# Kernel optimization log

Measured on AMD Instinct MI355X. Metric: run time of the kernel, lower is better.

## Reference

```python
import jax, jax.numpy as jnp
import numpy as np

H, D = 16, 64  # num_head, num_out
LN_EPS = 1e-5

def setup_inputs() -> dict:
    key = jax.random.key(0)
    ks = jax.random.split(key, 6)
    B, S, C = 4, 2048, 1024
    sc = 0.02
    return {
        "x": jax.random.normal(ks[0], (B, S, C), jnp.float32),
        "mask": jax.random.randint(ks[1], (B, S), 0, 2, jnp.int32),
        "Wq": jax.random.normal(ks[2], (C, C), jnp.float32) * sc,
        "Wk": jax.random.normal(ks[3], (C, C), jnp.float32) * sc,
        "Wv": jax.random.normal(ks[4], (C, C), jnp.float32) * sc,
        "Wr": jax.random.normal(ks[5], (C, C), jnp.float32) * sc,
        "gamma": jnp.ones((C,), jnp.float32),
        "beta": jnp.zeros((C,), jnpip := jnp.float32) if False else jnp.zeros((C,), jnp.float32),
    }

def reference(x, mask, Wq, Wk, Wv, Wr, gamma, beta):
    B, S, C = x.shape
    # torch Linear: y = x @ W.T ; split(num_out,-1) == reshape (B,S,H,D)
    q = (x @ Wq.T).reshape(B, S, H, D)
    k = (x @ Wk.T).reshape(B, S, H, D)
    v = (x @ Wv.T).reshape(B, S, H, D)
    scores = jnp.einsum("bqhd,bkhd->bhqk", q, k) / jnp.sqrt(jnp.float32(D))
    # mask [B,S] over keys; masked positions -> -1e9 (matches masked_fill)
    scores = jnp.where((mask == 0)[:, None, None, :], jnp.float32(-1e9), scores)
    attn = jax.nn.softmax(scores, axis=-1)
    out = jnp.einsum("bhqk,bkhd->bqhd", attn, v).reshape(B, S, H * D)
    out = jax.nn.relu(out + x @ Wr.T)
    mu = jnp.mean(out, axis=-1, keepdims=True)
    var = jnp.mean(jnp.square(out - mu), axis=-1, keepdims=True)
    return (out - mu) / jnp.sqrt(var + LN_EPS) * gamma + beta
```

## Files before the change

### kernel.cpp

```cpp
#include <hip/hip_runtime.h>

typedef __attribute__((ext_vector_type(8))) short short8;
typedef __attribute__((ext_vector_type(4))) float f32x4;
typedef __attribute__((ext_vector_type(4))) unsigned short u16x4;
typedef __attribute__((ext_vector_type(4))) float float4v;

#define MFMA(a, b, c) __builtin_amdgcn_mfma_f32_16x16x32_bf16(a, b, c, 0, 0, 0)
#define GLOAD_LDS16(gp, lp) __builtin_amdgcn_global_load_lds( \
    (const __attribute__((address_space(1))) void*)(gp),      \
    (__attribute__((address_space(3))) void*)(lp), 16, 0, 0)

__device__ __forceinline__ float bf2f(unsigned short u) {
    union { unsigned int i; float f; } v; v.i = ((unsigned int)u) << 16; return v.f;
}
__device__ __forceinline__ unsigned short f2bf(float f) {
    union { float f; unsigned int i; } v; v.f = f;
    unsigned int r = (v.i + 0x7FFFu + ((v.i >> 16) & 1u)) >> 16;
    return (unsigned short)r;
}
__device__ __forceinline__ unsigned short f2bfr(float f) {
    union { float f; unsigned int i; } v; v.f = f;
    return (unsigned short)((v.i + 0x8000u) >> 16);
}

__global__ __launch_bounds__(256)
void mask_scan(const int* __restrict__ mask, int* __restrict__ kidx, int* __restrict__ seff)
{
    constexpr int S = 2048;
    const int b = blockIdx.x;
    const int tid = threadIdx.x;
    __shared__ int ps[256];
    const int* m = mask + b * S;
    int loc[8], s = 0;
#pragma unroll
    for (int j = 0; j < 8; ++j) { loc[j] = m[tid * 8 + j]; s += loc[j]; }
#pragma unroll
    for (int j = 0; j < 8; ++j) kidx[b * S + tid * 8 + j] = b * S;
    ps[tid] = s;
    __syncthreads();
    for (int off = 1; off < 256; off <<= 1) {
        int v = (tid >= off) ? ps[tid - off] : 0;
        __syncthreads();
        ps[tid] += v;
        __syncthreads();
    }
    int run = (tid > 0) ? ps[tid - 1] : 0;
#pragma unroll
    for (int j = 0; j < 8; ++j) {
        if (loc[j]) kidx[b * S + run] = b * S + tid * 8 + j;
        run += loc[j];
    }
    if (tid == 255) seff[b] = ps[255];
}

__global__ __launch_bounds__(256)
void ingest(const float* __restrict__ src, unsigned short* __restrict__ dst, int n4)
{
    const int stride = gridDim.x * blockDim.x;
    for (int i = blockIdx.x * blockDim.x + threadIdx.x; i < n4; i += stride) {
        float4v v = ((const float4v*)src)[i];
        u16x4 o;
#pragma unroll
        for (int j = 0; j < 4; ++j) o[j] = f2bf(v[j]);
        ((u16x4*)dst)[i] = o;
    }
}

__global__ __launch_bounds__(256)
void proj_gemm(const unsigned short* __restrict__ X,
               const unsigned short* __restrict__ Wq, const unsigned short* __restrict__ Wk,
               const unsigned short* __restrict__ Wv, const unsigned short* __restrict__ Wr,
               unsigned short* __restrict__ Qo, unsigned short* __restrict__ Ko,
               unsigned short* __restrict__ Vo, unsigned short* __restrict__ Ro,
               const int* __restrict__ kidx, const int* __restrict__ seff)
{
    constexpr int Kd = 1024, N = 1024;
    __shared__ unsigned short As[128 * 32];
    __shared__ unsigned short Bs[128 * 32];
    const int tid = threadIdx.x;
    const int wid = tid >> 6, lane = tid & 63;
    const int g = lane >> 4, lr = lane & 15;
    const int wsel = blockIdx.z;
    const bool compact = (wsel == 1) || (wsel == 2);
    int rowBase;
    if (compact) {
        int bx = blockIdx.x;
        int b = bx / 17, xt = bx - b * 17;
        if (xt * 128 >= seff[b]) return;
        rowBase = b * 2048 + xt * 128;
    } else {
        if (blockIdx.x >= 64) return;
        rowBase = blockIdx.x * 128;
    }
    const unsigned short* W = (wsel == 0) ? Wq : (wsel == 1) ? Wk : (wsel == 2) ? Wv : Wr;
    unsigned short* O = (wsel == 0) ? Qo : (wsel == 1) ? Ko : (wsel == 2) ? Vo : Ro;
    const int colBase = blockIdx.y * 128;
    const int wm = wid >> 1, wn = wid & 1;

    f32x4 acc[4][4] = {};

    const int r0 = tid >> 2;
    const int c0 = (tid & 3) * 8;
    const int sA0 = compact ? kidx[rowBase + r0] : rowBase + r0;
    const int sA1 = compact ? kidx[rowBase + 64 + r0] : rowBase + 64 + r0;
    const unsigned short* ga0 = X + (size_t)sA0 * Kd + c0;
    const unsigned short* ga1 = X + (size_t)sA1 * Kd + c0;
    const unsigned short* gb0 = W + (size_t)(colBase + r0) * Kd + c0;
    const unsigned short* gb1 = W + (size_t)(colBase + 64 + r0) * Kd + c0;

    for (int kt = 0; kt < Kd; kt += 32) {
        if (kt) __syncthreads();
        GLOAD_LDS16(ga0 + kt, As + (size_t)tid * 8);
        GLOAD_LDS16(ga1 + kt, As + 2048 + (size_t)tid * 8);
        GLOAD_LDS16(gb0 + kt, Bs + (size_t)tid * 8);
        GLOAD_LDS16(gb1 + kt, Bs + 2048 + (size_t)tid * 8);
        asm volatile("s_waitcnt vmcnt(0)" ::: "memory");
        __syncthreads();
        short8 a[4], b[4];
#pragma unroll
        for (int mt = 0; mt < 4; ++mt)
            a[mt] = *reinterpret_cast<const short8*>(&As[(wm * 64 + mt * 16 + lr) * 32 + g * 8]);
#pragma unroll
        for (int nt = 0; nt < 4; ++nt)
            b[nt] = *reinterpret_cast<const short8*>(&Bs[(wn * 64 + nt * 16 + lr) * 32 + g * 8]);
#pragma unroll
        for (int mt = 0; mt < 4; ++mt)
#pragma unroll
            for (int nt = 0; nt < 4; ++nt)
                acc[mt][nt] = MFMA(a[mt], b[nt], acc[mt][nt]);
    }
#pragma unroll
    for (int mt = 0; mt < 4; ++mt)
#pragma unroll
        for (int nt = 0; nt < 4; ++nt)
#pragma unroll
            for (int r = 0; r < 4; ++r) {
                int row = rowBase + wm * 64 + mt * 16 + g * 4 + r;
                int col = colBase + wn * 64 + nt * 16 + lr;
                O[(size_t)row * N + col] = f2bf(acc[mt][nt][r]);
            }
}

__global__ __launch_bounds__(512)
void attn_fwd(const unsigned short* __restrict__ Q, const unsigned short* __restrict__ Kb,
              const unsigned short* __restrict__ Vb, const int* __restrict__ seff,
              unsigned short* __restrict__ AO)
{
    constexpr int S = 2048, C = 1024, Dh = 64;
    constexpr int PST = 64;
    constexpr float SCL = 0.125f * 1.44269504f;
    constexpr float FM  = 16.0f;
    constexpr float MSK = -1.0e30f;
    __shared__ unsigned short Kt[2][64 * 64];
    __shared__ unsigned short Vt[2][64 * 64];
    __shared__ unsigned short Pt[8][16 * PST];
    const int tid = threadIdx.x;
    const int w = tid >> 6, lane = tid & 63;
    const int g = lane >> 4, lr = lane & 15;
    const int lin = blockIdx.x;
    const int hb = lin & 63, qt = lin >> 6;
    const int h = hb >> 2, b = hb & 3;
    const int qbase = qt * 128;
    const int qrow = qbase + w * 16 + lr;

    const int Sb = seff[b];
    const int ntiles = (Sb + 63) >> 6;

    const unsigned short* qptr = Q + (size_t)(b * S + qrow) * C + h * Dh;
    short8 qf[2];
    qf[0] = *reinterpret_cast<const short8*>(qptr + g * 8);
    qf[1] = *reinterpret_cast<const short8*>(qptr + 32 + g * 8);

    short8 ones;
#pragma unroll
    for (int j = 0; j < 8; ++j) ones[j] = (short)0x3F80;

    f32x4 o[4] = {};
    f32x4 lacc = {};

    const unsigned short* kg = Kb + (size_t)(b * S) * C + h * Dh;
    const unsigned short* vg = Vb + (size_t)(b * S) * C + h * Dh;

    const int kk0 = tid >> 3;
    const int kd0 = ((tid & 7) ^ (kk0 & 7)) * 8;
    const int vkey = tid >> 3;
    const int vsd = (tid & 7) * 8;

    short8 vv;
    GLOAD_LDS16(kg + (size_t)kk0 * C + kd0, &Kt[0][(size_t)tid * 8]);
    vv = *reinterpret_cast<const short8*>(vg + (size_t)vkey * C + vsd);
    asm volatile("s_waitcnt vmcnt(0)" ::: "memory");
    {
        const unsigned short* bb = (const unsigned short*)&vv;
#pragma unroll
        for (int j = 0; j < 8; ++j) {
            int d = vsd + j;
            int sw = (d & 7) ^ ((d >> 3) & 7);
            Vt[0][d * 64 + ((((vkey >> 3) ^ sw) << 3) | (vkey & 7))] = bb[j];
        }
    }
    __syncthreads();

    int cur = 0;
    for (int tt = 0; tt < ntiles; ++tt) {
        const int t = tt * 64;
        const bool hasNext = (tt + 1) < ntiles;
        if (hasNext) {
            const int tn = t + 64;
            GLOAD_LDS16(kg + (size_t)(tn + kk0) * C + kd0, &Kt[cur ^ 1][(size_t)tid * 8]);
            vv = *reinterpret_cast<const short8*>(vg + (size_t)(tn + vkey) * C + vsd);
        }
        f32x4 s[4];
        __builtin_amdgcn_s_setprio(1);
#pragma unroll
        for (int nt = 0; nt < 4; ++nt) {
            int key = nt * 16 + lr;
            f32x4 a = {};
#pragma unroll
            for (int c = 0; c < 2; ++c) {
                int dd = c * 32 + g * 8;
                short8 kf = *reinterpret_cast<const short8*>(
                    &Kt[cur][key * 64 + (((dd >> 3) ^ (key & 7)) << 3)]);
                a = MFMA(qf[c], kf, a);
            }
            s[nt] = a;
        }
        __builtin_amdgcn_s_setprio(0);
        float madd[4];
#pragma unroll
        for (int nt = 0; nt < 4; ++nt)
            madd[nt] = ((t + nt * 16 + lr) < Sb) ? -FM : MSK;
        unsigned short* Pw = Pt[w];
#pragma unroll
        for (int nt = 0; nt < 4; ++nt) {
            int k = nt * 16 + lr;
#pragma unroll
            for (int r = 0; r < 4; ++r) {
                float p = __builtin_amdgcn_exp2f(s[nt][r] * SCL + madd[nt]);
                int row = g * 4 + r;
                Pw[row * PST + ((((k >> 3) ^ (row & 7)) << 3) | (k & 7))] = f2bfr(p);
            }
        }
        asm volatile("s_waitcnt lgkmcnt(0)" ::: "memory");
        __builtin_amdgcn_sched_barrier(0);
        short8 pf[2];
#pragma unroll
        for (int hh = 0; hh < 2; ++hh) {
            int kk = hh * 32 + g * 8;
            pf[hh] = *reinterpret_cast<const short8*>(
                &Pw[lr * PST + (((kk >> 3) ^ (lr & 7)) << 3)]);
        }
        __builtin_amdgcn_s_setprio(1);
        lacc = MFMA(pf[0], ones, lacc);
        lacc = MFMA(pf[1], ones, lacc);
#pragma unroll
        for (int dt = 0; dt < 4; ++dt) {
            int d = dt * 16 + lr;
#pragma unroll
            for (int hh = 0; hh < 2; ++hh) {
                int kk = hh * 32 + g * 8;
                short8 vf = *reinterpret_cast<const short8*>(
                    &Vt[cur][d * 64 + ((((kk >> 3) ^ (d & 7) ^ ((d >> 3) & 7)) << 3))]);
                o[dt] = MFMA(pf[hh], vf, o[dt]);
            }
        }
        __builtin_amdgcn_s_setprio(0);
        if (hasNext) {
            asm volatile("s_waitcnt vmcnt(0)" ::: "memory");
            const unsigned short* bb = (const unsigned short*)&vv;
            unsigned short* Vn = Vt[cur ^ 1];
#pragma unroll
            for (int j = 0; j < 8; ++j) {
                int d = vsd + j;
                int sw = (d & 7) ^ ((d >> 3) & 7);
                Vn[d * 64 + ((((vkey >> 3) ^ sw) << 3) | (vkey & 7))] = bb[j];
            }
        }
        __syncthreads();
        cur ^= 1;
    }
#pragma unroll
    for (int dt = 0; dt < 4; ++dt)
#pragma unroll
        for (int r = 0; r < 4; ++r) {
            int row = qbase + w * 16 + g * 4 + r;
            int col = h * Dh + dt * 16 + lr;
            AO[(size_t)(b * S + row) * C + col] = f2bf(o[dt][r] / lacc[r]);
        }
}

__global__ __launch_bounds__(256)
void ln_ep(const unsigned short* __restrict__ AO, const unsigned short* __restrict__ R,
           const float* __restrict__ gamma, const float* __restrict__ beta,
           float* __restrict__ out)
{
    constexpr int C = 1024;
    const int row = blockIdx.x;
    const int tid = threadIdx.x;
    __shared__ float s1[256];
    __shared__ float s2[256];

    float v[4]; float sum = 0.f, ss = 0.f;
#pragma unroll
    for (int i = 0; i < 4; ++i) {
        int c = tid * 4 + i;
        float a = bf2f(AO[(size_t)row * C + c]);
        float r = bf2f(R[(size_t)row * C + c]);
        v[i] = fmaxf(0.f, a + r);
        sum += v[i]; ss += v[i] * v[i];
    }
    s1[tid] = sum; s2[tid] = ss;
    __syncthreads();
    for (int st = 128; st > 0; st >>= 1) {
        if (tid < st) { s1[tid] += s1[tid + st]; s2[tid] += s2[tid + st]; }
        __syncthreads();
    }
    float mu = s1[0] * (1.f / C);
    float var = s2[0] * (1.f / C) - mu * mu;
    float rstd = rsqrtf(var + 1e-5f);
    float4v g4 = *reinterpret_cast<const float4v*>(gamma + tid * 4);
    float4v b4 = *reinterpret_cast<const float4v*>(beta + tid * 4);
    float4v ov;
#pragma unroll
    for (int i = 0; i < 4; ++i)
        ov[i] = (v[i] - mu) * rstd * g4[i] + b4[i];
    *reinterpret_cast<float4v*>(out + (size_t)row * C + tid * 4) = ov;
}

extern "C" void kernel_launch(void* const* d_in, const int* in_sizes, int n_in,
                              void* d_out, int out_size, void* d_ws, size_t ws_size,
                              hipStream_t stream)
{
    const float* X = (const float*)d_in[0];
    const int* mask = (const int*)d_in[1];
    const float* Wq = (const float*)d_in[2];
    const float* Wk = (const float*)d_in[3];
    const float* Wv = (const float*)d_in[4];
    const float* Wr = (const float*)d_in[5];
    const float* Gm = (const float*)d_in[6];
    const float* Bt = (const float*)d_in[7];
    float* out = (float*)d_out;

    const size_t NE = (size_t)8192 * 1024;
    const size_t WE = (size_t)1024 * 1024;
    unsigned short* p = (unsigned short*)d_ws;
    unsigned short* Xb = p;   p += NE;
    unsigned short* Wqb = p;  p += WE;
    unsigned short* Wkb = p;  p += WE;
    unsigned short* Wvb = p;  p += WE;
    unsigned short* Wrb = p;  p += WE;
    unsigned short* Qb = p;   p += NE;
    unsigned short* Kb = p;   p += NE;
    unsigned short* Vb = p;   p += NE;
    unsigned short* Rb = p;   p += NE;
    int* kidx = (int*)p;      p += 8192 * 2;
    int* seff = (int*)p;      p += 8;
    unsigned short* AO = Xb;

    mask_scan<<<dim3(4), 256, 0, stream>>>(mask, kidx, seff);
    ingest<<<dim3(2048), 256, 0, stream>>>(X, Xb, (int)(NE / 4));
    ingest<<<dim3(512), 256, 0, stream>>>(Wq, Wqb, (int)(WE / 4));
    ingest<<<dim3(512), 256, 0, stream>>>(Wk, Wkb, (int)(WE / 4));
    ingest<<<dim3(512), 256, 0, stream>>>(Wv, Wvb, (int)(WE / 4));
    ingest<<<dim3(512), 256, 0, stream>>>(Wr, Wrb, (int)(WE / 4));

    proj_gemm<<<dim3(68, 8, 4), 256, 0, stream>>>(Xb, Wqb, Wkb, Wvb, Wrb,
                                                  Qb, Kb, Vb, Rb, kidx, seff);
    attn_fwd<<<dim3(1024), 512, 0, stream>>>(Qb, Kb, Vb, seff, AO);
    ln_ep<<<dim3(8192), 256, 0, stream>>>(AO, Rb, Gm, Bt, out);
}
```

Before: 177.2 us.

## Fuse ingest launches, swizzle projection grid, and coalesce GEMM stores via LDS

Merges the five fp32-to-bf16 conversion launches into one kernel writing the contiguous workspace. Flattens the projection GEMM grid to a 1D index grouped so eight row tiles share weight column tiles, aiming for better cache reuse. Stages the output tile through padded shared memory so global stores become 16-byte coalesced rows instead of scattered 2-byte writes. The extra shared buffer raises LDS use per block, which may lower occupancy.

```diff
diff --git a/kernel.cpp b/kernel.cpp
--- a/kernel.cpp
+++ b/kernel.cpp
@@ -1,6 +1,7 @@
 #include <hip/hip_runtime.h>
 
 typedef __attribute__((ext_vector_type(8))) short short8;
+typedef __attribute__((ext_vector_type(8))) unsigned short u16x8;
 typedef __attribute__((ext_vector_type(4))) float f32x4;
 typedef __attribute__((ext_vector_type(4))) unsigned short u16x4;
 typedef __attribute__((ext_vector_type(4))) float float4v;
@@ -54,11 +55,25 @@
 }
 
 __global__ __launch_bounds__(256)
-void ingest(const float* __restrict__ src, unsigned short* __restrict__ dst, int n4)
-{
+void ingest_all(const float* __restrict__ X,
+                const float* __restrict__ Wq, const float* __restrict__ Wk,
+                const float* __restrict__ Wv, const float* __restrict__ Wr,
+                unsigned short* __restrict__ dst)
+{
+    constexpr int X4 = 2097152;
+    constexpr int T4 = X4 + 4 * 262144;
     const int stride = gridDim.x * blockDim.x;
-    for (int i = blockIdx.x * blockDim.x + threadIdx.x; i < n4; i += stride) {
-        float4v v = ((const float4v*)src)[i];
+    for (int i = blockIdx.x * blockDim.x + threadIdx.x; i < T4; i += stride) {
+        const float* src;
+        int off;
+        if (i < X4) { src = X; off = i; }
+        else {
+            int jj = i - X4;
+            int ws = jj >> 18;
+            off = jj & 0x3FFFF;
+            src = (ws == 0) ? Wq : (ws == 1) ? Wk : (ws == 2) ? Wv : Wr;
+        }
+        float4v v = ((const float4v*)src)[off];
         u16x4 o;
 #pragma unroll
         for (int j = 0; j < 4; ++j) o[j] = f2bf(v[j]);
@@ -77,24 +92,30 @@
     constexpr int Kd = 1024, N = 1024;
     __shared__ unsigned short As[128 * 32];
     __shared__ unsigned short Bs[128 * 32];
+    __shared__ unsigned short Ct[128 * 136];
     const int tid = threadIdx.x;
     const int wid = tid >> 6, lane = tid & 63;
     const int g = lane >> 4, lr = lane & 15;
-    const int wsel = blockIdx.z;
+    const int bid = blockIdx.x;
+    const int jx = bid & 7, t = bid >> 3;
+    const int x = (t >> 5) * 8 + jx;
+    const int c = t & 31;
+    const int wsel = c >> 3;
+    const int coltile = c & 7;
     const bool compact = (wsel == 1) || (wsel == 2);
     int rowBase;
     if (compact) {
-        int bx = blockIdx.x;
-        int b = bx / 17, xt = bx - b * 17;
+        if (x >= 68) return;
+        int b = x / 17, xt = x - b * 17;
         if (xt * 128 >= seff[b]) return;
         rowBase = b * 2048 + xt * 128;
     } else {
-        if (blockIdx.x >= 64) return;
-        rowBase = blockIdx.x * 128;
+        if (x >= 64) return;
+        rowBase = x * 128;
     }
     const unsigned short* W = (wsel == 0) ? Wq : (wsel == 1) ? Wk : (wsel == 2) ? Wv : Wr;
     unsigned short* O = (wsel == 0) ? Qo : (wsel == 1) ? Ko : (wsel == 2) ? Vo : Ro;
-    const int colBase = blockIdx.y * 128;
+    const int colBase = coltile * 128;
     const int wm = wid >> 1, wn = wid & 1;
 
     f32x4 acc[4][4] = {};
@@ -134,11 +155,17 @@
 #pragma unroll
         for (int nt = 0; nt < 4; ++nt)
 #pragma unroll
-            for (int r = 0; r < 4; ++r) {
-                int row = rowBase + wm * 64 + mt * 16 + g * 4 + r;
-                int col = colBase + wn * 64 + nt * 16 + lr;
-                O[(size_t)row * N + col] = f2bf(acc[mt][nt][r]);
-            }
+            for (int r = 0; r < 4; ++r)
+                Ct[(wm * 64 + mt * 16 + g * 4 + r) * 136 + wn * 64 + nt * 16 + lr] =
+                    f2bf(acc[mt][nt][r]);
+    __syncthreads();
+#pragma unroll
+    for (int pp = 0; pp < 8; ++pp) {
+        int row = pp * 16 + (tid >> 4);
+        int col = (tid & 15) * 8;
+        u16x8 v8 = *reinterpret_cast<const u16x8*>(&Ct[row * 136 + col]);
+        *reinterpret_cast<u16x8*>(&O[(size_t)(rowBase + row) * N + colBase + col]) = v8;
+    }
 }
 
 __global__ __launch_bounds__(512)
@@ -358,14 +385,10 @@
     unsigned short* AO = Xb;
 
     mask_scan<<<dim3(4), 256, 0, stream>>>(mask, kidx, seff);
-    ingest<<<dim3(2048), 256, 0, stream>>>(X, Xb, (int)(NE / 4));
-    ingest<<<dim3(512), 256, 0, stream>>>(Wq, Wqb, (int)(WE / 4));
-    ingest<<<dim3(512), 256, 0, stream>>>(Wk, Wkb, (int)(WE / 4));
-    ingest<<<dim3(512), 256, 0, stream>>>(Wv, Wvb, (int)(WE / 4));
-    ingest<<<dim3(512), 256, 0, stream>>>(Wr, Wrb, (int)(WE / 4));
-
-    proj_gemm<<<dim3(68, 8, 4), 256, 0, stream>>>(Xb, Wqb, Wkb, Wvb, Wrb,
-                                                  Qb, Kb, Vb, Rb, kidx, seff);
+    ingest_all<<<dim3(2048), 256, 0, stream>>>(X, Wq, Wk, Wv, Wr, Xb);
+
+    proj_gemm<<<dim3(2304), 256, 0, stream>>>(Xb, Wqb, Wkb, Wvb, Wrb,
+                                              Qb, Kb, Vb, Rb, kidx, seff);
     attn_fwd<<<dim3(1024), 512, 0, stream>>>(Qb, Kb, Vb, seff, AO);
     ln_ep<<<dim3(8192), 256, 0, stream>>>(AO, Rb, Gm, Bt, out);
 }
```

After: 171.5 us. 3.2% less time.
